# Optimization experiments

Hardware: AMD Instinct MI355X
Metric: run time of the kernel (lower is better)

## Reference

```python
import jax, jax.numpy as jnp
import numpy as np

N_PFAS, N_GW, N_SW = 20000, 100000, 30000
D, OUT = 128, 128
E_PG, E_GP, E_PS, E_SP = 1600000, 640000, 480000, 320000


def setup_inputs() -> dict:
    key = jax.random.key(0)
    ks = jax.random.split(key, 32)
    g = lambda k, shape, fan_in: jax.random.normal(k, shape, jnp.float32) / np.sqrt(fan_in)
    inp = {
        "x_pfas": jax.random.normal(ks[0], (N_PFAS, D), jnp.float32),
        "x_gw": jax.random.normal(ks[1], (N_GW, D), jnp.float32),
        "x_sw": jax.random.normal(ks[2], (N_SW, D), jnp.float32),
        "ei_pg_src": jax.random.randint(ks[3], (E_PG,), 0, N_PFAS),
        "ei_pg_dst": jax.random.randint(ks[4], (E_PG,), 0, N_GW),
        "ei_gp_src": jax.random.randint(ks[5], (E_GP,), 0, N_GW),
        "ei_gp_dst": jax.random.randint(ks[6], (E_GP,), 0, N_PFAS),
        "ei_ps_src": jax.random.randint(ks[7], (E_PS,), 0, N_PFAS),
        "ei_ps_dst": jax.random.randint(ks[8], (E_PS,), 0, N_SW),
        "ei_sp_src": jax.random.randint(ks[9], (E_SP,), 0, N_SW),
        "ei_sp_dst": jax.random.randint(ks[10], (E_SP,), 0, N_PFAS),
    }
    # SAGEConv params per relation: lin_l (on aggregated neighbors, with bias), lin_r (root, no bias)
    names = ["pg", "gp", "ps", "sp"]
    for i, n in enumerate(names):
        inp[f"Wl_{n}"] = g(ks[11 + 3 * i], (D, OUT), D)
        inp[f"bl_{n}"] = jnp.zeros((OUT,), jnp.float32)
        inp[f"Wr_{n}"] = g(ks[12 + 3 * i], (D, OUT), D)
    inp["W_gw"] = g(ks[25], (OUT, 1), OUT)
    inp["b_gw"] = jnp.zeros((1,), jnp.float32)
    inp["W_sw"] = g(ks[26], (OUT, 1), OUT)
    inp["b_sw"] = jnp.zeros((1,), jnp.float32)
    return inp


def _sage(x_src, x_dst, src, dst, n_dst, Wl, bl, Wr):
    # SAGEConv: lin_l(mean_j x_src[j]) + lin_r(x_dst)
    msg = x_src[src]  # [E, D] gather
    s = jax.ops.segment_sum(msg, dst, num_segments=n_dst)
    cnt = jax.ops.segment_sum(jnp.ones((src.shape[0],), x_src.dtype), dst, num_segments=n_dst)
    mean = s / jnp.maximum(cnt, 1.0)[:, None]
    return mean @ Wl + bl + x_dst @ Wr


def reference(x_pfas, x_gw, x_sw,
              ei_pg_src, ei_pg_dst, ei_gp_src, ei_gp_dst,
              ei_ps_src, ei_ps_dst, ei_sp_src, ei_sp_dst,
              Wl_pg, bl_pg, Wr_pg, Wl_gp, bl_gp, Wr_gp,
              Wl_ps, bl_ps, Wr_ps, Wl_sp, bl_sp, Wr_sp,
              W_gw, b_gw, W_sw, b_sw):
    h_gw = _sage(x_pfas, x_gw, ei_pg_src, ei_pg_dst, N_GW, Wl_pg, bl_pg, Wr_pg)
    h_sw = _sage(x_pfas, x_sw, ei_ps_src, ei_ps_dst, N_SW, Wl_ps, bl_ps, Wr_ps)
    # pfas_sites is the destination of two relations -> HeteroConv aggr='sum'
    h_pf = (_sage(x_gw, x_pfas, ei_gp_src, ei_gp_dst, N_PFAS, Wl_gp, bl_gp, Wr_gp)
            + _sage(x_sw, x_pfas, ei_sp_src, ei_sp_dst, N_PFAS, Wl_sp, bl_sp, Wr_sp))
    h_pf = jax.nn.relu(h_pf)
    h_gw = jax.nn.relu(h_gw)
    h_sw = jax.nn.relu(h_sw)
    out_gw = h_gw @ W_gw + b_gw   # [N_GW, 1]
    out_sw = h_sw @ W_sw + b_sw   # [N_SW, 1]
    return h_pf, out_gw, out_sw
```

## Files before the change

### kernel.cpp

```cpp
#include <hip/hip_runtime.h>

#define N_PFAS 20000
#define N_GW   100000
#define N_SW   30000
#define E_PG   1600000
#define E_GP   640000
#define E_PS   480000
#define E_SP   320000
#define E_TOT  (E_PG + E_PS + E_GP + E_SP)
#define BASE_PG 0
#define BASE_PS (N_GW)
#define BASE_GP (N_GW + N_SW)
#define BASE_SP (N_GW + N_SW + N_PFAS)
#define NTOT    (N_GW + N_SW + 2 * N_PFAS)
#define NB        ((NTOT + 255) / 256)
#define BIN_EPT   12
#define BIN_EPB   (1024 * BIN_EPT)
#define BIN_NBLK  ((E_TOT + BIN_EPB - 1) / BIN_EPB)
#define SEG_CAP   15360
#define H_NBLK    128
#define T64_PF ((N_PFAS + 63) / 64)
#define T64_GW ((N_GW + 63) / 64)
#define T64_SW ((N_SW + 63) / 64)
#define T64_ALL (T64_PF + T64_GW + T64_SW)
#define GW_BLKS   ((N_GW + 63) / 64)
#define SW_BLKS   ((N_SW + 63) / 64)
#define SEGP_BLKS (N_PFAS / 16)

typedef _Float16 h2_t  __attribute__((ext_vector_type(2)));
typedef _Float16 f16x8 __attribute__((ext_vector_type(8)));
typedef float    f32x4 __attribute__((ext_vector_type(4)));
union HU { unsigned u; h2_t h; };
__device__ __forceinline__ h2_t u2h2(unsigned u) { HU x; x.u = u; return x.h; }

__device__ __forceinline__ void gather_sum_f16(
    const unsigned short* __restrict__ bufT16, const int* __restrict__ perm,
    int lo, int hi, int tx, h2_t& tl, h2_t& th)
{
    h2_t hz; hz.x = (_Float16)0.f; hz.y = (_Float16)0.f;
    h2_t a0 = hz, a1 = hz, a2 = hz, a3 = hz, a4 = hz, a5 = hz, a6 = hz, a7 = hz;
    int i = lo;
    for (; i + 8 <= hi; i += 8) {
        uint2 v0 = *(const uint2*)(bufT16 + (size_t)perm[i + 0] * 128 + tx * 4);
        uint2 v1 = *(const uint2*)(bufT16 + (size_t)perm[i + 1] * 128 + tx * 4);
        uint2 v2 = *(const uint2*)(bufT16 + (size_t)perm[i + 2] * 128 + tx * 4);
        uint2 v3 = *(const uint2*)(bufT16 + (size_t)perm[i + 3] * 128 + tx * 4);
        uint2 v4 = *(const uint2*)(bufT16 + (size_t)perm[i + 4] * 128 + tx * 4);
        uint2 v5 = *(const uint2*)(bufT16 + (size_t)perm[i + 5] * 128 + tx * 4);
        uint2 v6 = *(const uint2*)(bufT16 + (size_t)perm[i + 6] * 128 + tx * 4);
        uint2 v7 = *(const uint2*)(bufT16 + (size_t)perm[i + 7] * 128 + tx * 4);
        a0 += u2h2(v0.x); a1 += u2h2(v0.y);
        a2 += u2h2(v1.x); a3 += u2h2(v1.y);
        a4 += u2h2(v2.x); a5 += u2h2(v2.y);
        a6 += u2h2(v3.x); a7 += u2h2(v3.y);
        a0 += u2h2(v4.x); a1 += u2h2(v4.y);
        a2 += u2h2(v5.x); a3 += u2h2(v5.y);
        a4 += u2h2(v6.x); a5 += u2h2(v6.y);
        a6 += u2h2(v7.x); a7 += u2h2(v7.y);
    }
    for (; i + 2 <= hi; i += 2) {
        uint2 v0 = *(const uint2*)(bufT16 + (size_t)perm[i + 0] * 128 + tx * 4);
        uint2 v1 = *(const uint2*)(bufT16 + (size_t)perm[i + 1] * 128 + tx * 4);
        a0 += u2h2(v0.x); a1 += u2h2(v0.y);
        a2 += u2h2(v1.x); a3 += u2h2(v1.y);
    }
    if (i < hi) {
        uint2 v0 = *(const uint2*)(bufT16 + (size_t)perm[i] * 128 + tx * 4);
        a0 += u2h2(v0.x); a1 += u2h2(v0.y);
    }
    tl = (a0 + a2) + (a4 + a6);
    th = (a1 + a3) + (a5 + a7);
}

__global__ __launch_bounds__(256) void prep_wt_kernel(
    const float* __restrict__ Wl_pg, const float* __restrict__ Wl_ps,
    const float* __restrict__ Wr_gp, const float* __restrict__ Wr_sp,
    const float* __restrict__ Wl_gp, const float* __restrict__ Wr_pg,
    const float* __restrict__ Wl_sp, const float* __restrict__ Wr_ps,
    _Float16* __restrict__ WtF_pg, _Float16* __restrict__ WtF_ps,
    _Float16* __restrict__ WtFR_pf,
    _Float16* __restrict__ WtF_gp, _Float16* __restrict__ WtFR_gw,
    _Float16* __restrict__ WtF_sp, _Float16* __restrict__ WtFR_sw)
{
    const int m = blockIdx.x;
    const float* A = nullptr; const float* B = nullptr; _Float16* O = nullptr;
    switch (m) {
        case 0: A = Wl_pg; O = WtF_pg;  break;
        case 1: A = Wl_ps; O = WtF_ps;  break;
        case 2: A = Wr_gp; B = Wr_sp; O = WtFR_pf; break;
        case 3: A = Wl_gp; O = WtF_gp;  break;
        case 4: A = Wr_pg; O = WtFR_gw; break;
        case 5: A = Wl_sp; O = WtF_sp;  break;
        default: A = Wr_ps; O = WtFR_sw; break;
    }
    for (int t = threadIdx.x; t < 2048; t += 256) {
        int lane = t & 63, g = t >> 6;
        int ks = g & 3, ct = g >> 2;
        int nn = ct * 16 + (lane & 15);
        int k0 = ks * 32 + (lane >> 4) * 8;
        f16x8 v;
#pragma unroll
        for (int j = 0; j < 8; ++j) {
            float x = A[(k0 + j) * 128 + nn];
            if (B) x += B[(k0 + j) * 128 + nn];
            v[j] = (_Float16)x;
        }
        *(f16x8*)(O + (size_t)t * 8) = v;
    }
}

template<bool F16OUT>
__device__ __forceinline__ void mfma_one_B(
    const _Float16* __restrict__ WtF, const f16x8* a,
    int rbase, int n, int lane,
    _Float16* __restrict__ o16, float* __restrict__ o32)
{
    f16x8 bf[8][4];
#pragma unroll
    for (int ct = 0; ct < 8; ++ct)
#pragma unroll
        for (int ks = 0; ks < 4; ++ks)
            bf[ct][ks] = *(const f16x8*)(WtF + (size_t)((ct * 4 + ks) * 64 + lane) * 8);

    f32x4 acc[8];
#pragma unroll
    for (int ct = 0; ct < 8; ++ct) acc[ct] = (f32x4){0.f, 0.f, 0.f, 0.f};
#pragma unroll
    for (int ct = 0; ct < 8; ++ct)
#pragma unroll
        for (int ks = 0; ks < 4; ++ks)
            acc[ct] = __builtin_amdgcn_mfma_f32_16x16x32_f16(a[ks], bf[ct][ks], acc[ct], 0, 0, 0);

    const int rowb = rbase + (lane >> 4) * 4;
    const int bcol = lane & 15;
#pragma unroll
    for (int ct = 0; ct < 8; ++ct) {
        const int col = ct * 16 + bcol;
#pragma unroll
        for (int e = 0; e < 4; ++e) {
            int r = rowb + e;
            if (r < n) {
                if (F16OUT) o16[((size_t)r << 7) + col] = (_Float16)acc[ct][e];
                else        o32[((size_t)r << 7) + col] = acc[ct][e];
            }
        }
    }
}

__global__ __launch_bounds__(256, 2) void mfma_trans_kernel(
    const float* __restrict__ x_pfas, const float* __restrict__ x_gw,
    const float* __restrict__ x_sw,
    const _Float16* __restrict__ WtF_pg, const _Float16* __restrict__ WtF_ps,
    const _Float16* __restrict__ WtFR_pf,
    const _Float16* __restrict__ WtF_gp, const _Float16* __restrict__ WtFR_gw,
    const _Float16* __restrict__ WtF_sp, const _Float16* __restrict__ WtFR_sw,
    _Float16* __restrict__ bufT_pg, _Float16* __restrict__ bufT_ps,
    float* __restrict__ R_pf,
    _Float16* __restrict__ bufT_gp, _Float16* __restrict__ R_gw,
    _Float16* __restrict__ bufT_sp, _Float16* __restrict__ R_sw)
{
    const int b = blockIdx.x;
    int mode, tile, n; const float* X;
    if (b < T64_PF)               { mode = 0; tile = b;                    X = x_pfas; n = N_PFAS; }
    else if (b < T64_PF + T64_GW) { mode = 1; tile = b - T64_PF;           X = x_gw;   n = N_GW; }
    else                          { mode = 2; tile = b - T64_PF - T64_GW;  X = x_sw;   n = N_SW; }
    const int lane = threadIdx.x & 63;
    const int w    = threadIdx.x >> 6;
    const int rbase = tile * 64 + w * 16;
    const int rA = rbase + (lane & 15);
    const int ko = (lane >> 4) * 8;

    f16x8 a[4];
#pragma unroll
    for (int ks = 0; ks < 4; ++ks) {
        float4 x0 = make_float4(0.f, 0.f, 0.f, 0.f), x1 = x0;
        if (rA < n) {
            const float* xp = X + ((size_t)rA << 7) + ks * 32 + ko;
            x0 = *(const float4*)xp;
            x1 = *(const float4*)(xp + 4);
        }
        f16x8 v;
        v[0] = (_Float16)x0.x; v[1] = (_Float16)x0.y; v[2] = (_Float16)x0.z; v[3] = (_Float16)x0.w;
        v[4] = (_Float16)x1.x; v[5] = (_Float16)x1.y; v[6] = (_Float16)x1.z; v[7] = (_Float16)x1.w;
        a[ks] = v;
    }
    if (mode == 0) {
        mfma_one_B<true >(WtF_pg,  a, rbase, n, lane, bufT_pg, nullptr);
        mfma_one_B<true >(WtF_ps,  a, rbase, n, lane, bufT_ps, nullptr);
        mfma_one_B<false>(WtFR_pf, a, rbase, n, lane, nullptr, R_pf);
    } else if (mode == 1) {
        mfma_one_B<true>(WtF_gp,  a, rbase, n, lane, bufT_gp, nullptr);
        mfma_one_B<true>(WtFR_gw, a, rbase, n, lane, R_gw,    nullptr);
    } else {
        mfma_one_B<true>(WtF_sp,  a, rbase, n, lane, bufT_sp, nullptr);
        mfma_one_B<true>(WtFR_sw, a, rbase, n, lane, R_sw,    nullptr);
    }
}

__global__ __launch_bounds__(512, 8) void gather_all_kernel(
    const _Float16* __restrict__ R_gw, const _Float16* __restrict__ R_sw,
    const float* __restrict__ bl_pg, const float* __restrict__ bl_ps,
    const unsigned short* __restrict__ bufT_pg,
    const unsigned short* __restrict__ bufT_ps,
    const unsigned short* __restrict__ bufT_gp,
    const unsigned short* __restrict__ bufT_sp,
    const int* __restrict__ perm, const int* __restrict__ off_all,
    const float* __restrict__ W_gw, const float* __restrict__ b_gw,
    const float* __restrict__ W_sw, const float* __restrict__ b_sw,
    float* __restrict__ o_gw, float* __restrict__ o_sw,
    float* __restrict__ contrib_gp, float* __restrict__ contrib_sp)
{
    const int b = blockIdx.x;
    const int tid = threadIdx.x;
    const int tx = tid & 31;
    const int g = tid >> 5;

    if (b < GW_BLKS + SW_BLKS) {
        int n; const _Float16* R; const float* bl; const unsigned short* bufT16;
        const int* off; const float* wout; const float* bout; float* out; int tile;
        if (b < GW_BLKS) {
            n = N_GW; R = R_gw; bl = bl_pg; bufT16 = bufT_pg; off = off_all + BASE_PG;
            wout = W_gw; bout = b_gw; out = o_gw; tile = b;
        } else {
            n = N_SW; R = R_sw; bl = bl_ps; bufT16 = bufT_ps; off = off_all + BASE_PS;
            wout = W_sw; bout = b_sw; out = o_sw; tile = b - GW_BLKS;
        }
        const int rbase = tile * 64 + g * 4;
        float4 bv = ((const float4*)bl)[tx];
        float4 wo = ((const float4*)wout)[tx];
        float bo = bout[0];
#pragma unroll
        for (int rr = 0; rr < 4; ++rr) {
            int r = rbase + rr;
            int lo = 0, hi = 0;
            if (r < n) { lo = off[r]; hi = off[r + 1]; }
            h2_t tl, th;
            gather_sum_f16(bufT16, perm, lo, hi, tx, tl, th);
            float4 rf = make_float4(0.f, 0.f, 0.f, 0.f);
            if (r < n) {
                uint2 rv = *(const uint2*)((const unsigned short*)R + ((size_t)r << 7) + tx * 4);
                h2_t r01 = u2h2(rv.x), r23 = u2h2(rv.y);
                rf = make_float4((float)r01.x, (float)r01.y, (float)r23.x, (float)r23.y);
            }
            float inv = 1.0f / fmaxf((float)(hi - lo), 1.0f);
            float h0  = fmaxf(rf.x + bv.x + (float)tl.x * inv, 0.f);
            float h1  = fmaxf(rf.y + bv.y + (float)tl.y * inv, 0.f);
            float h2v = fmaxf(rf.z + bv.z + (float)th.x * inv, 0.f);
            float h3  = fmaxf(rf.w + bv.w + (float)th.y * inv, 0.f);
            float pv = h0 * wo.x + h1 * wo.y + h2v * wo.z + h3 * wo.w;
            pv += __shfl_xor(pv, 1, 32);
            pv += __shfl_xor(pv, 2, 32);
            pv += __shfl_xor(pv, 4, 32);
            pv += __shfl_xor(pv, 8, 32);
            pv += __shfl_xor(pv, 16, 32);
            if (tx == 0 && r < n) out[r] = pv + bo;
        }
    } else {
        const int b2 = b - (GW_BLKS + SW_BLKS);
        const unsigned short* bufT; const int* off; float* contrib; int node;
        if (b2 < SEGP_BLKS) {
            bufT = bufT_gp; off = off_all + BASE_GP; contrib = contrib_gp; node = b2 * 16 + g;
        } else {
            bufT = bufT_sp; off = off_all + BASE_SP; contrib = contrib_sp; node = (b2 - SEGP_BLKS) * 16 + g;
        }
        int lo = off[node], hi = off[node + 1];
        h2_t tl, th;
        gather_sum_f16(bufT, perm, lo, hi, tx, tl, th);
        float inv = 1.0f / fmaxf((float)(hi - lo), 1.0f);
        float4 o;
        o.x = (float)tl.x * inv; o.y = (float)tl.y * inv;
        o.z = (float)th.x * inv; o.w = (float)th.y * inv;
        ((float4*)contrib)[(size_t)node * 32 + tx] = o;
    }
}

__global__ __launch_bounds__(256) void pf_final_kernel(
    const float* __restrict__ R_pf,
    const float* __restrict__ contrib_gp, const float* __restrict__ contrib_sp,
    const float* __restrict__ blG, const float* __restrict__ blS,
    float* __restrict__ out)
{
    int t = blockIdx.x * 256 + threadIdx.x;
    if (t >= N_PFAS * 32) return;
    int c4 = t & 31;
    float4 b1 = ((const float4*)blG)[c4];
    float4 b2 = ((const float4*)blS)[c4];
    float4 rv = ((const float4*)R_pf)[t];
    float4 cg = ((const float4*)contrib_gp)[t];
    float4 cs = ((const float4*)contrib_sp)[t];
    float4 o;
    o.x = fmaxf(rv.x + cg.x + cs.x + b1.x + b2.x, 0.f);
    o.y = fmaxf(rv.y + cg.y + cs.y + b1.y + b2.y, 0.f);
    o.z = fmaxf(rv.z + cg.z + cs.z + b1.z + b2.z, 0.f);
    o.w = fmaxf(rv.w + cg.w + cs.w + b1.w + b2.w, 0.f);
    ((float4*)out)[t] = o;
}

__global__ __launch_bounds__(1024) void bucket_hist_kernel(
    const int* __restrict__ d_pg, const int* __restrict__ d_ps,
    const int* __restrict__ d_gp, const int* __restrict__ d_sp,
    int* __restrict__ bucketCounts)
{
    __shared__ int hist[NB];
    const int tid = threadIdx.x;
    for (int i = tid; i < NB; i += 1024) hist[i] = 0;
    __syncthreads();
    for (int e = blockIdx.x * 1024 + tid; e < E_TOT; e += H_NBLK * 1024) {
        int idx;
        if (e < E_PG)                    idx = BASE_PG + d_pg[e];
        else if (e < E_PG + E_PS)        idx = BASE_PS + d_ps[e - E_PG];
        else if (e < E_PG + E_PS + E_GP) idx = BASE_GP + d_gp[e - E_PG - E_PS];
        else                             idx = BASE_SP + d_sp[e - E_PG - E_PS - E_GP];
        atomicAdd(&hist[idx >> 8], 1);
    }
    __syncthreads();
    for (int i = tid; i < NB; i += 1024) {
        int c = hist[i];
        if (c) atomicAdd(&bucketCounts[i], c);
    }
}

__global__ __launch_bounds__(1024) void bucket_scan_kernel(
    const int* __restrict__ bucketCounts, int* __restrict__ bucketOff,
    int* __restrict__ gcursor, int* __restrict__ off_all)
{
    __shared__ int sp[1024];
    const int t = threadIdx.x;
    int v = (t < NB) ? bucketCounts[t] : 0;
    sp[t] = v;
    __syncthreads();
    for (int ofs = 1; ofs < 1024; ofs <<= 1) {
        int add = (t >= ofs) ? sp[t - ofs] : 0;
        __syncthreads();
        sp[t] += add;
        __syncthreads();
    }
    if (t < NB) {
        int excl = sp[t] - v;
        bucketOff[t] = excl;
        gcursor[t] = excl;
    }
    if (t == 0) { bucketOff[NB] = E_TOT; off_all[NTOT] = E_TOT; }
}

__global__ __launch_bounds__(1024) void bin_kernel(
    const int* __restrict__ s_pg, const int* __restrict__ d_pg,
    const int* __restrict__ s_ps, const int* __restrict__ d_ps,
    const int* __restrict__ s_gp, const int* __restrict__ d_gp,
    const int* __restrict__ s_sp, const int* __restrict__ d_sp,
    int* __restrict__ gcursor, unsigned* __restrict__ pairs)
{
    __shared__ int hist[NB];
    __shared__ int chunkBase[NB];
    const int tid = threadIdx.x;
    for (int i = tid; i < NB; i += 1024) hist[i] = 0;
    __syncthreads();

    const int base = blockIdx.x * BIN_EPB;
    int bkt[BIN_EPT], rnk[BIN_EPT];
    unsigned pk[BIN_EPT];
#pragma unroll
    for (int k = 0; k < BIN_EPT; ++k) {
        int e = base + k * 1024 + tid;
        int idx = -1, src = 0;
        if (e < E_PG) { idx = BASE_PG + d_pg[e]; src = s_pg[e]; }
        else if (e < E_PG + E_PS) { int i2 = e - E_PG; idx = BASE_PS + d_ps[i2]; src = s_ps[i2]; }
        else if (e < E_PG + E_PS + E_GP) { int i2 = e - E_PG - E_PS; idx = BASE_GP + d_gp[i2]; src = s_gp[i2]; }
        else if (e < E_TOT) { int i2 = e - E_PG - E_PS - E_GP; idx = BASE_SP + d_sp[i2]; src = s_sp[i2]; }
        if (idx >= 0) {
            int b = idx >> 8;
            bkt[k] = b;
            rnk[k] = atomicAdd(&hist[b], 1);
            pk[k] = (unsigned)(idx & 255) | ((unsigned)src << 8);
        } else bkt[k] = -1;
    }
    __syncthreads();
    for (int i = tid; i < NB; i += 1024) {
        int c = hist[i];
        chunkBase[i] = c ? atomicAdd(&gcursor[i], c) : 0;
    }
    __syncthreads();
#pragma unroll
    for (int k = 0; k < BIN_EPT; ++k)
        if (bkt[k] >= 0) pairs[chunkBase[bkt[k]] + rnk[k]] = pk[k];
}

__global__ __launch_bounds__(1024) void unbin_kernel(
    const unsigned* __restrict__ pairs, const int* __restrict__ bucketOff,
    int* __restrict__ off_all, int* __restrict__ perm_all)
{
    __shared__ int sPerm[SEG_CAP];
    __shared__ int cnt[256];
    __shared__ int sp[256];
    __shared__ int cur[256];
    const int b = blockIdx.x;
    const int nb0 = b << 8;
    const int nb1 = min(nb0 + 256, NTOT);
    const int tid = threadIdx.x;
    const int base = bucketOff[b];
    const int end  = bucketOff[b + 1];
    const int len = end - base;

    if (tid < 256) cnt[tid] = 0;
    __syncthreads();
    for (int i = base + tid; i < end; i += 1024)
        atomicAdd(&cnt[pairs[i] & 255u], 1);
    __syncthreads();
    int v = (tid < 256) ? cnt[tid] : 0;
    if (tid < 256) sp[tid] = v;
    __syncthreads();
    for (int ofs = 1; ofs < 256; ofs <<= 1) {
        int add = (tid < 256 && tid >= ofs) ? sp[tid - ofs] : 0;
        __syncthreads();
        if (tid < 256) sp[tid] += add;
        __syncthreads();
    }
    if (tid < 256) {
        int excl = sp[tid] - v;
        cur[tid] = excl;
        if (nb0 + tid < nb1) off_all[nb0 + tid] = base + excl;
    }
    __syncthreads();

    if (len <= SEG_CAP) {
        for (int i = base + tid; i < end; i += 1024) {
            unsigned p = pairs[i];
            int pos = atomicAdd(&cur[p & 255u], 1);
            sPerm[pos] = (int)(p >> 8);
        }
        __syncthreads();
        for (int i = tid; i < len; i += 1024)
            perm_all[base + i] = sPerm[i];
    } else {
        for (int i = base + tid; i < end; i += 1024) {
            unsigned p = pairs[i];
            int pos = atomicAdd(&cur[p & 255u], 1);
            perm_all[base + pos] = (int)(p >> 8);
        }
    }
}

extern "C" void kernel_launch(void* const* d_in, const int* in_sizes, int n_in,
                              void* d_out, int out_size, void* d_ws, size_t ws_size,
                              hipStream_t stream)
{
    const float* x_pfas = (const float*)d_in[0];
    const float* x_gw   = (const float*)d_in[1];
    const float* x_sw   = (const float*)d_in[2];
    const int* ei_pg_src = (const int*)d_in[3];
    const int* ei_pg_dst = (const int*)d_in[4];
    const int* ei_gp_src = (const int*)d_in[5];
    const int* ei_gp_dst = (const int*)d_in[6];
    const int* ei_ps_src = (const int*)d_in[7];
    const int* ei_ps_dst = (const int*)d_in[8];
    const int* ei_sp_src = (const int*)d_in[9];
    const int* ei_sp_dst = (const int*)d_in[10];
    const float* Wl_pg = (const float*)d_in[11];
    const float* bl_pg = (const float*)d_in[12];
    const float* Wr_pg = (const float*)d_in[13];
    const float* Wl_gp = (const float*)d_in[14];
    const float* bl_gp = (const float*)d_in[15];
    const float* Wr_gp = (const float*)d_in[16];
    const float* Wl_ps = (const float*)d_in[17];
    const float* bl_ps = (const float*)d_in[18];
    const float* Wr_ps = (const float*)d_in[19];
    const float* Wl_sp = (const float*)d_in[20];
    const float* bl_sp = (const float*)d_in[21];
    const float* Wr_sp = (const float*)d_in[22];
    const float* W_gw = (const float*)d_in[23];
    const float* b_gw = (const float*)d_in[24];
    const float* W_sw = (const float*)d_in[25];
    const float* b_sw = (const float*)d_in[26];

    float* out  = (float*)d_out;
    float* h_pf = out;
    float* o_gw = out + (size_t)N_PFAS * 128;
    float* o_sw = o_gw + N_GW;

    char* p = (char*)d_ws;
    auto alloc = [&](size_t bytes) { char* q = p; p += (bytes + 15) & ~(size_t)15; return q; };
    unsigned short* bufT_pg = (unsigned short*)alloc((size_t)N_PFAS * 128 * 2);
    unsigned short* bufT_ps = (unsigned short*)alloc((size_t)N_PFAS * 128 * 2);
    unsigned short* bufT_gp = (unsigned short*)alloc((size_t)N_GW * 128 * 2);
    unsigned short* bufT_sp = (unsigned short*)alloc((size_t)N_SW * 128 * 2);
    _Float16* R_gw = (_Float16*)alloc((size_t)N_GW * 128 * 2);
    _Float16* R_sw = (_Float16*)alloc((size_t)N_SW * 128 * 2);
    float* R_pf = (float*)alloc((size_t)N_PFAS * 128 * 4);
    float* contrib_gp = (float*)alloc((size_t)N_PFAS * 128 * 4);
    float* contrib_sp = (float*)alloc((size_t)N_PFAS * 128 * 4);
    int* perm_all   = (int*)alloc((size_t)E_TOT * 4);
    unsigned* pairs = (unsigned*)alloc((size_t)E_TOT * 4);
    int* off_all    = (int*)alloc((size_t)(NTOT + 1) * 4);
    int* bucketCounts = (int*)alloc((size_t)NB * 4);
    int* bucketOff    = (int*)alloc((size_t)(NB + 1) * 4);
    int* gcursor    = (int*)alloc((size_t)NB * 4);
    _Float16* WtF_pg  = (_Float16*)alloc(16384 * 2);
    _Float16* WtF_ps  = (_Float16*)alloc(16384 * 2);
    _Float16* WtFR_pf = (_Float16*)alloc(16384 * 2);
    _Float16* WtF_gp  = (_Float16*)alloc(16384 * 2);
    _Float16* WtFR_gw = (_Float16*)alloc(16384 * 2);
    _Float16* WtF_sp  = (_Float16*)alloc(16384 * 2);
    _Float16* WtFR_sw = (_Float16*)alloc(16384 * 2);

    prep_wt_kernel<<<7, 256, 0, stream>>>(
        Wl_pg, Wl_ps, Wr_gp, Wr_sp, Wl_gp, Wr_pg, Wl_sp, Wr_ps,
        WtF_pg, WtF_ps, WtFR_pf, WtF_gp, WtFR_gw, WtF_sp, WtFR_sw);
    mfma_trans_kernel<<<T64_ALL, 256, 0, stream>>>(
        x_pfas, x_gw, x_sw,
        WtF_pg, WtF_ps, WtFR_pf, WtF_gp, WtFR_gw, WtF_sp, WtFR_sw,
        (_Float16*)bufT_pg, (_Float16*)bufT_ps, R_pf,
        (_Float16*)bufT_gp, R_gw, (_Float16*)bufT_sp, R_sw);

    hipMemsetAsync(bucketCounts, 0, (size_t)NB * 4, stream);
    bucket_hist_kernel<<<H_NBLK, 1024, 0, stream>>>(
        ei_pg_dst, ei_ps_dst, ei_gp_dst, ei_sp_dst, bucketCounts);
    bucket_scan_kernel<<<1, 1024, 0, stream>>>(
        bucketCounts, bucketOff, gcursor, off_all);
    bin_kernel<<<BIN_NBLK, 1024, 0, stream>>>(
        ei_pg_src, ei_pg_dst, ei_ps_src, ei_ps_dst,
        ei_gp_src, ei_gp_dst, ei_sp_src, ei_sp_dst, gcursor, pairs);
    unbin_kernel<<<NB, 1024, 0, stream>>>(pairs, bucketOff, off_all, perm_all);

    gather_all_kernel<<<GW_BLKS + SW_BLKS + 2 * SEGP_BLKS, 512, 0, stream>>>(
        R_gw, R_sw, bl_pg, bl_ps, bufT_pg, bufT_ps, bufT_gp, bufT_sp,
        perm_all, off_all, W_gw, b_gw, W_sw, b_sw, o_gw, o_sw,
        contrib_gp, contrib_sp);

    pf_final_kernel<<<(N_PFAS * 32 + 255) / 256, 256, 0, stream>>>(
        R_pf, contrib_gp, contrib_sp, bl_gp, bl_sp, h_pf);
}
```

Baseline: 383.6 us.

## Fuse bucket histogram into transform kernel, stage f16 stores via LDS

```diff
diff --git a/kernel.cpp b/kernel.cpp
--- a/kernel.cpp
+++ b/kernel.cpp
@@ -14,18 +14,19 @@
 #define BASE_SP (N_GW + N_SW + N_PFAS)
 #define NTOT    (N_GW + N_SW + 2 * N_PFAS)
 #define NB        ((NTOT + 255) / 256)
-#define BIN_EPT   12
-#define BIN_EPB   (1024 * BIN_EPT)
+#define BIN_EPT   8
+#define BIN_EPB   (512 * BIN_EPT)
 #define BIN_NBLK  ((E_TOT + BIN_EPB - 1) / BIN_EPB)
-#define SEG_CAP   15360
-#define H_NBLK    128
+#define SEG_CAP   9216
 #define T64_PF ((N_PFAS + 63) / 64)
 #define T64_GW ((N_GW + 63) / 64)
 #define T64_SW ((N_SW + 63) / 64)
 #define T64_ALL (T64_PF + T64_GW + T64_SW)
+#define TH_HIST_BLKS 512
 #define GW_BLKS   ((N_GW + 63) / 64)
 #define SW_BLKS   ((N_SW + 63) / 64)
 #define SEGP_BLKS (N_PFAS / 16)
+#define SSTR 136
 
 typedef _Float16 h2_t  __attribute__((ext_vector_type(2)));
 typedef _Float16 f16x8 __attribute__((ext_vector_type(8)));
@@ -80,9 +81,13 @@
     _Float16* __restrict__ WtF_pg, _Float16* __restrict__ WtF_ps,
     _Float16* __restrict__ WtFR_pf,
     _Float16* __restrict__ WtF_gp, _Float16* __restrict__ WtFR_gw,
-    _Float16* __restrict__ WtF_sp, _Float16* __restrict__ WtFR_sw)
+    _Float16* __restrict__ WtF_sp, _Float16* __restrict__ WtFR_sw,
+    int* __restrict__ bucketCounts)
 {
     const int m = blockIdx.x;
+    if (m == 0) {
+        for (int i = threadIdx.x; i < NB; i += 256) bucketCounts[i] = 0;
+    }
     const float* A = nullptr; const float* B = nullptr; _Float16* O = nullptr;
     switch (m) {
         case 0: A = Wl_pg; O = WtF_pg;  break;
@@ -109,11 +114,9 @@
     }
 }
 
-template<bool F16OUT>
-__device__ __forceinline__ void mfma_one_B(
-    const _Float16* __restrict__ WtF, const f16x8* a,
-    int rbase, int n, int lane,
-    _Float16* __restrict__ o16, float* __restrict__ o32)
+__device__ __forceinline__ void mfma_one_B16(
+    const _Float16* __restrict__ WtF, const f16x8* a, _Float16* sstage,
+    int rbase, int n, int lane, _Float16* __restrict__ o16)
 {
     f16x8 bf[8][4];
 #pragma unroll
@@ -131,6 +134,43 @@
         for (int ks = 0; ks < 4; ++ks)
             acc[ct] = __builtin_amdgcn_mfma_f32_16x16x32_f16(a[ks], bf[ct][ks], acc[ct], 0, 0, 0);
 
+    const int rl = (lane >> 4) * 4;
+    const int cb = lane & 15;
+#pragma unroll
+    for (int ct = 0; ct < 8; ++ct)
+#pragma unroll
+        for (int e = 0; e < 4; ++e)
+            sstage[(rl + e) * SSTR + ct * 16 + cb] = (_Float16)acc[ct][e];
+
+#pragma unroll
+    for (int i = 0; i < 4; ++i) {
+        int lr = i * 4 + (lane >> 4);
+        int r = rbase + lr;
+        if (r < n) {
+            f16x8 v = *(const f16x8*)(sstage + lr * SSTR + cb * 8);
+            *(f16x8*)(o16 + ((size_t)r << 7) + cb * 8) = v;
+        }
+    }
+}
+
+__device__ __forceinline__ void mfma_one_B32(
+    const _Float16* __restrict__ WtF, const f16x8* a,
+    int rbase, int n, int lane, float* __restrict__ o32)
+{
+    f16x8 bf[8][4];
+#pragma unroll
+    for (int ct = 0; ct < 8; ++ct)
+#pragma unroll
+        for (int ks = 0; ks < 4; ++ks)
+            bf[ct][ks] = *(const f16x8*)(WtF + (size_t)((ct * 4 + ks) * 64 + lane) * 8);
+    f32x4 acc[8];
+#pragma unroll
+    for (int ct = 0; ct < 8; ++ct) acc[ct] = (f32x4){0.f, 0.f, 0.f, 0.f};
+#pragma unroll
+    for (int ct = 0; ct < 8; ++ct)
+#pragma unroll
+        for (int ks = 0; ks < 4; ++ks)
+            acc[ct] = __builtin_amdgcn_mfma_f32_16x16x32_f16(a[ks], bf[ct][ks], acc[ct], 0, 0, 0);
     const int rowb = rbase + (lane >> 4) * 4;
     const int bcol = lane & 15;
 #pragma unroll
@@ -139,15 +179,12 @@
 #pragma unroll
         for (int e = 0; e < 4; ++e) {
             int r = rowb + e;
-            if (r < n) {
-                if (F16OUT) o16[((size_t)r << 7) + col] = (_Float16)acc[ct][e];
-                else        o32[((size_t)r << 7) + col] = acc[ct][e];
-            }
-        }
-    }
-}
-
-__global__ __launch_bounds__(256, 2) void mfma_trans_kernel(
+            if (r < n) o32[((size_t)r << 7) + col] = acc[ct][e];
+        }
+    }
+}
+
+__global__ __launch_bounds__(256, 2) void trans_hist_kernel(
     const float* __restrict__ x_pfas, const float* __restrict__ x_gw,
     const float* __restrict__ x_sw,
     const _Float16* __restrict__ WtF_pg, const _Float16* __restrict__ WtF_ps,
@@ -157,18 +194,45 @@
     _Float16* __restrict__ bufT_pg, _Float16* __restrict__ bufT_ps,
     float* __restrict__ R_pf,
     _Float16* __restrict__ bufT_gp, _Float16* __restrict__ R_gw,
-    _Float16* __restrict__ bufT_sp, _Float16* __restrict__ R_sw)
-{
-    const int b = blockIdx.x;
+    _Float16* __restrict__ bufT_sp, _Float16* __restrict__ R_sw,
+    const int* __restrict__ d_pg, const int* __restrict__ d_ps,
+    const int* __restrict__ d_gp, const int* __restrict__ d_sp,
+    int* __restrict__ bucketCounts)
+{
+    __shared__ char smem[4 * 16 * SSTR * 2];
+    const int tid = threadIdx.x;
+
+    if (blockIdx.x < TH_HIST_BLKS) {
+        int* hist = (int*)smem;
+        for (int i = tid; i < NB; i += 256) hist[i] = 0;
+        __syncthreads();
+        for (int e = blockIdx.x * 256 + tid; e < E_TOT; e += TH_HIST_BLKS * 256) {
+            int idx;
+            if (e < E_PG)                    idx = BASE_PG + d_pg[e];
+            else if (e < E_PG + E_PS)        idx = BASE_PS + d_ps[e - E_PG];
+            else if (e < E_PG + E_PS + E_GP) idx = BASE_GP + d_gp[e - E_PG - E_PS];
+            else                             idx = BASE_SP + d_sp[e - E_PG - E_PS - E_GP];
+            atomicAdd(&hist[idx >> 8], 1);
+        }
+        __syncthreads();
+        for (int i = tid; i < NB; i += 256) {
+            int c = hist[i];
+            if (c) atomicAdd(&bucketCounts[i], c);
+        }
+        return;
+    }
+
+    const int b = blockIdx.x - TH_HIST_BLKS;
     int mode, tile, n; const float* X;
     if (b < T64_PF)               { mode = 0; tile = b;                    X = x_pfas; n = N_PFAS; }
     else if (b < T64_PF + T64_GW) { mode = 1; tile = b - T64_PF;           X = x_gw;   n = N_GW; }
     else                          { mode = 2; tile = b - T64_PF - T64_GW;  X = x_sw;   n = N_SW; }
-    const int lane = threadIdx.x & 63;
-    const int w    = threadIdx.x >> 6;
+    const int lane = tid & 63;
+    const int w    = tid >> 6;
     const int rbase = tile * 64 + w * 16;
     const int rA = rbase + (lane & 15);
     const int ko = (lane >> 4) * 8;
+    _Float16* sstage = (_Float16*)smem + (size_t)w * 16 * SSTR;
 
     f16x8 a[4];
 #pragma unroll
@@ -185,15 +249,15 @@
         a[ks] = v;
     }
     if (mode == 0) {
-        mfma_one_B<true >(WtF_pg,  a, rbase, n, lane, bufT_pg, nullptr);
-        mfma_one_B<true >(WtF_ps,  a, rbase, n, lane, bufT_ps, nullptr);
-        mfma_one_B<false>(WtFR_pf, a, rbase, n, lane, nullptr, R_pf);
+        mfma_one_B16(WtF_pg,  a, sstage, rbase, n, lane, bufT_pg);
+        mfma_one_B16(WtF_ps,  a, sstage, rbase, n, lane, bufT_ps);
+        mfma_one_B32(WtFR_pf, a, rbase, n, lane, R_pf);
     } else if (mode == 1) {
-        mfma_one_B<true>(WtF_gp,  a, rbase, n, lane, bufT_gp, nullptr);
-        mfma_one_B<true>(WtFR_gw, a, rbase, n, lane, R_gw,    nullptr);
+        mfma_one_B16(WtF_gp,  a, sstage, rbase, n, lane, bufT_gp);
+        mfma_one_B16(WtFR_gw, a, sstage, rbase, n, lane, R_gw);
     } else {
-        mfma_one_B<true>(WtF_sp,  a, rbase, n, lane, bufT_sp, nullptr);
-        mfma_one_B<true>(WtFR_sw, a, rbase, n, lane, R_sw,    nullptr);
+        mfma_one_B16(WtF_sp,  a, sstage, rbase, n, lane, bufT_sp);
+        mfma_one_B16(WtFR_sw, a, sstage, rbase, n, lane, R_sw);
     }
 }
 
@@ -296,30 +360,6 @@
     ((float4*)out)[t] = o;
 }
 
-__global__ __launch_bounds__(1024) void bucket_hist_kernel(
-    const int* __restrict__ d_pg, const int* __restrict__ d_ps,
-    const int* __restrict__ d_gp, const int* __restrict__ d_sp,
-    int* __restrict__ bucketCounts)
-{
-    __shared__ int hist[NB];
-    const int tid = threadIdx.x;
-    for (int i = tid; i < NB; i += 1024) hist[i] = 0;
-    __syncthreads();
-    for (int e = blockIdx.x * 1024 + tid; e < E_TOT; e += H_NBLK * 1024) {
-        int idx;
-        if (e < E_PG)                    idx = BASE_PG + d_pg[e];
-        else if (e < E_PG + E_PS)        idx = BASE_PS + d_ps[e - E_PG];
-        else if (e < E_PG + E_PS + E_GP) idx = BASE_GP + d_gp[e - E_PG - E_PS];
-        else                             idx = BASE_SP + d_sp[e - E_PG - E_PS - E_GP];
-        atomicAdd(&hist[idx >> 8], 1);
-    }
-    __syncthreads();
-    for (int i = tid; i < NB; i += 1024) {
-        int c = hist[i];
-        if (c) atomicAdd(&bucketCounts[i], c);
-    }
-}
-
 __global__ __launch_bounds__(1024) void bucket_scan_kernel(
     const int* __restrict__ bucketCounts, int* __restrict__ bucketOff,
     int* __restrict__ gcursor, int* __restrict__ off_all)
@@ -343,7 +383,7 @@
     if (t == 0) { bucketOff[NB] = E_TOT; off_all[NTOT] = E_TOT; }
 }
 
-__global__ __launch_bounds__(1024) void bin_kernel(
+__global__ __launch_bounds__(512) void bin_kernel(
     const int* __restrict__ s_pg, const int* __restrict__ d_pg,
     const int* __restrict__ s_ps, const int* __restrict__ d_ps,
     const int* __restrict__ s_gp, const int* __restrict__ d_gp,
@@ -353,7 +393,7 @@
     __shared__ int hist[NB];
     __shared__ int chunkBase[NB];
     const int tid = threadIdx.x;
-    for (int i = tid; i < NB; i += 1024) hist[i] = 0;
+    for (int i = tid; i < NB; i += 512) hist[i] = 0;
     __syncthreads();
 
     const int base = blockIdx.x * BIN_EPB;
@@ -361,7 +401,7 @@
     unsigned pk[BIN_EPT];
 #pragma unroll
     for (int k = 0; k < BIN_EPT; ++k) {
-        int e = base + k * 1024 + tid;
+        int e = base + k * 512 + tid;
         int idx = -1, src = 0;
         if (e < E_PG) { idx = BASE_PG + d_pg[e]; src = s_pg[e]; }
         else if (e < E_PG + E_PS) { int i2 = e - E_PG; idx = BASE_PS + d_ps[i2]; src = s_ps[i2]; }
@@ -375,7 +415,7 @@
         } else bkt[k] = -1;
     }
     __syncthreads();
-    for (int i = tid; i < NB; i += 1024) {
+    for (int i = tid; i < NB; i += 512) {
         int c = hist[i];
         chunkBase[i] = c ? atomicAdd(&gcursor[i], c) : 0;
     }
@@ -385,7 +425,7 @@
         if (bkt[k] >= 0) pairs[chunkBase[bkt[k]] + rnk[k]] = pk[k];
 }
 
-__global__ __launch_bounds__(1024) void unbin_kernel(
+__global__ __launch_bounds__(512) void unbin_kernel(
     const unsigned* __restrict__ pairs, const int* __restrict__ bucketOff,
     int* __restrict__ off_all, int* __restrict__ perm_all)
 {
@@ -403,7 +443,7 @@
 
     if (tid < 256) cnt[tid] = 0;
     __syncthreads();
-    for (int i = base + tid; i < end; i += 1024)
+    for (int i = base + tid; i < end; i += 512)
         atomicAdd(&cnt[pairs[i] & 255u], 1);
     __syncthreads();
     int v = (tid < 256) ? cnt[tid] : 0;
@@ -423,16 +463,16 @@
     __syncthreads();
 
     if (len <= SEG_CAP) {
-        for (int i = base + tid; i < end; i += 1024) {
+        for (int i = base + tid; i < end; i += 512) {
             unsigned p = pairs[i];
             int pos = atomicAdd(&cur[p & 255u], 1);
             sPerm[pos] = (int)(p >> 8);
         }
         __syncthreads();
-        for (int i = tid; i < len; i += 1024)
+        for (int i = tid; i < len; i += 512)
             perm_all[base + i] = sPerm[i];
     } else {
-        for (int i = base + tid; i < end; i += 1024) {
+        for (int i = base + tid; i < end; i += 512) {
             unsigned p = pairs[i];
             int pos = atomicAdd(&cur[p & 255u], 1);
             perm_all[base + pos] = (int)(p >> 8);
@@ -504,22 +544,22 @@
 
     prep_wt_kernel<<<7, 256, 0, stream>>>(
         Wl_pg, Wl_ps, Wr_gp, Wr_sp, Wl_gp, Wr_pg, Wl_sp, Wr_ps,
-        WtF_pg, WtF_ps, WtFR_pf, WtF_gp, WtFR_gw, WtF_sp, WtFR_sw);
-    mfma_trans_kernel<<<T64_ALL, 256, 0, stream>>>(
+        WtF_pg, WtF_ps, WtFR_pf, WtF_gp, WtFR_gw, WtF_sp, WtFR_sw,
+        bucketCounts);
+
+    trans_hist_kernel<<<TH_HIST_BLKS + T64_ALL, 256, 0, stream>>>(
         x_pfas, x_gw, x_sw,
         WtF_pg, WtF_ps, WtFR_pf, WtF_gp, WtFR_gw, WtF_sp, WtFR_sw,
         (_Float16*)bufT_pg, (_Float16*)bufT_ps, R_pf,
-        (_Float16*)bufT_gp, R_gw, (_Float16*)bufT_sp, R_sw);
-
-    hipMemsetAsync(bucketCounts, 0, (size_t)NB * 4, stream);
-    bucket_hist_kernel<<<H_NBLK, 1024, 0, stream>>>(
+        (_Float16*)bufT_gp, R_gw, (_Float16*)bufT_sp, R_sw,
         ei_pg_dst, ei_ps_dst, ei_gp_dst, ei_sp_dst, bucketCounts);
+
     bucket_scan_kernel<<<1, 1024, 0, stream>>>(
         bucketCounts, bucketOff, gcursor, off_all);
-    bin_kernel<<<BIN_NBLK, 1024, 0, stream>>>(
+    bin_kernel<<<BIN_NBLK, 512, 0, stream>>>(
         ei_pg_src, ei_pg_dst, ei_ps_src, ei_ps_dst,
         ei_gp_src, ei_gp_dst, ei_sp_src, ei_sp_dst, gcursor, pairs);
-    unbin_kernel<<<NB, 1024, 0, stream>>>(pairs, bucketOff, off_all, perm_all);
+    unbin_kernel<<<NB, 512, 0, stream>>>(pairs, bucketOff, off_all, perm_all);
 
     gather_all_kernel<<<GW_BLKS + SW_BLKS + 2 * SEGP_BLKS, 512, 0, stream>>>(
         R_gw, R_sw, bl_pg, bl_ps, bufT_pg, bufT_ps, bufT_gp, bufT_sp,
```

Result: faster. 374.4 us (-2.4%).
